# Performance work log

Hardware: AMD Instinct MI355X
Metric: run time of the kernel (lower is better)

Reference implementation:

```python
import jax, jax.numpy as jnp
import numpy as np

B, D, H, O, E = 16384, 256, 256, 256, 32
N_ACTIVE = 22          # int(32 * 0.7) from BoltzmannGate
TEMP = float(np.e)     # Boltzmann temperature
EPS = 1e-8


def setup_inputs() -> dict:
    key = jax.random.key(0)
    ks = jax.random.split(key, 7)
    s = 0.02  # init scale for weights
    return {
        "x":  jax.random.normal(ks[0], (B, D), dtype=jnp.float32),
        "W1": jax.random.normal(ks[1], (E, H, D), dtype=jnp.float32) * s,  # [E, out=H, in=D] torch Linear layout
        "b1": jax.random.normal(ks[2], (E, H), dtype=jnp.float32) * s,
        "W2": jax.random.normal(ks[3], (E, O, H), dtype=jnp.float32) * s,
        "b2": jax.random.normal(ks[4], (E, O), dtype=jnp.float32) * s,
        "Wg": jax.random.normal(ks[5], (E, D), dtype=jnp.float32) * s,
        "bg": jax.random.normal(ks[6], (E,), dtype=jnp.float32) * s,
    }


def reference(x, W1, b1, W2, b2, Wg, bg):
    # Dense all-experts forward: [B, E, H] -> relu -> [B, E, O]
    h = jax.nn.relu(jnp.einsum('bd,ehd->beh', x, W1) + b1[None, :, :])
    expert_out = jnp.einsum('beh,eoh->beo', h, W2) + b2[None, :, :]

    # Boltzmann gate: softmax(scores / T), keep top-k probs, renormalize.
    scores = (x @ Wg.T + bg) / TEMP                      # [B, E]
    probs = jax.nn.softmax(scores, axis=-1)
    _, topk_idx = jax.lax.top_k(probs, N_ACTIVE)         # [B, N_ACTIVE]
    mask = jnp.zeros_like(probs).at[jnp.arange(B)[:, None], topk_idx].set(1.0)
    weights = probs * mask
    weights = weights / (jnp.sum(weights, axis=-1, keepdims=True) + EPS)

    # Weighted combine over experts: [B, O]
    return jnp.einsum('be,beo->bo', weights, expert_out)
```

## Files before the change

### kernel.cpp

```cpp
#include <hip/hip_runtime.h>
#include <hip/hip_bf16.h>


typedef __attribute__((ext_vector_type(8))) short bf16x8;
typedef __attribute__((ext_vector_type(4))) float f32x4;

__device__ __forceinline__ unsigned short f2bf(float f) {
    unsigned u = __builtin_bit_cast(unsigned, f);
    u += 0x7FFFu + ((u >> 16) & 1u);
    return (unsigned short)(u >> 16);
}
__device__ __forceinline__ unsigned pack_bf16x2(float a, float b) {
    return (unsigned)f2bf(a) | ((unsigned)f2bf(b) << 16);
}

#define LX(r, ch) (((r) << 8) + ((((ch) ^ ((r) & 7))) << 3))

__global__ __launch_bounds__(256) void cvt_w(const float* __restrict__ W1,
                                             const float* __restrict__ W2,
                                             unsigned short* __restrict__ Wr) {
    int T = blockIdx.x * 256 + threadIdx.x;
    int lane = T & 63, t = (T >> 6) & 3, kb = (T >> 8) & 7;
    int g = (T >> 11) & 7, e = T >> 14;
    int l15 = lane & 15, quad = lane >> 4;
    int row = (g & 3) * 64 + t * 16 + l15;
    const float* src = ((g < 4) ? W1 : W2) +
                       ((long)e * 256 + row) * 256 + kb * 32 + quad * 8;
    float4 v0 = ((const float4*)src)[0], v1 = ((const float4*)src)[1];
    uint4 o;
    o.x = pack_bf16x2(v0.x, v0.y); o.y = pack_bf16x2(v0.z, v0.w);
    o.z = pack_bf16x2(v1.x, v1.y); o.w = pack_bf16x2(v1.z, v1.w);
    ((uint4*)Wr)[T] = o;
}

__global__ __launch_bounds__(512, 2) void moe_kernel(
    const float* __restrict__ x,
    const unsigned short* __restrict__ Wr,
    const float* __restrict__ bias1,
    const float* __restrict__ b2,
    const float* __restrict__ Wg,
    const float* __restrict__ bg,
    float* __restrict__ out)
{
    __shared__ __align__(16) unsigned short x_s[64 * 256];
    __shared__ __align__(16) unsigned short h_s[64 * 256];
    __shared__ float gws[64 * 33];

    const int tid  = threadIdx.x;
    const int wv   = tid >> 6, lane = tid & 63;
    const int quad = lane >> 4, l15 = lane & 15;
    const int crew = wv >> 2, g = wv & 3;
    const int row0 = blockIdx.x * 64;

#pragma unroll
    for (int c = 0; c < 4; ++c) {
        int chunk = tid + c * 512;
        int r = chunk >> 5, ch = chunk & 31;
        const float4* s = (const float4*)(x + (long)(row0 + r) * 256 + ch * 8);
        float4 v0 = s[0], v1 = s[1];
        uint4 o;
        o.x = pack_bf16x2(v0.x, v0.y); o.y = pack_bf16x2(v0.z, v0.w);
        o.z = pack_bf16x2(v1.x, v1.y); o.w = pack_bf16x2(v1.z, v1.w);
        *(uint4*)(&x_s[LX(r, ch)]) = o;
    }

    {
        const int e32 = lane & 31, half = lane >> 5;
        const float4* wg4 = (const float4*)(Wg + e32 * 256 + half * 128);
        float bgv = bg[e32];
        for (int i = 0; i < 8; ++i) {
            int lr = wv * 8 + i;
            const float4* xr4 = (const float4*)(x + (long)(row0 + lr) * 256 + half * 128);
            float acc = 0.f;
#pragma unroll
            for (int tt = 0; tt < 32; ++tt) {
                float4 w = wg4[tt], xv = xr4[tt];
                acc = fmaf(w.x, xv.x, acc); acc = fmaf(w.y, xv.y, acc);
                acc = fmaf(w.z, xv.z, acc); acc = fmaf(w.w, xv.w, acc);
            }
            acc += __shfl_xor(acc, 32);
            float score = (acc + bgv) / 2.71828182845904523f;

            float m = score;
#pragma unroll
            for (int d = 16; d >= 1; d >>= 1) m = fmaxf(m, __shfl_xor(m, d));
            float p = expf(score - m);
            float ps = p;
#pragma unroll
            for (int d = 16; d >= 1; d >>= 1) ps += __shfl_xor(ps, d);
            float prob = p / ps;

            int rank = 0;
#pragma unroll
            for (int j = 0; j < 32; ++j) {
                float pj = __shfl(prob, j);
                rank += (pj > prob || (pj == prob && j < e32)) ? 1 : 0;
            }
            float kept = (rank < 22) ? prob : 0.f;
            float wsum = kept;
#pragma unroll
            for (int d = 16; d >= 1; d >>= 1) wsum += __shfl_xor(wsum, d);
            float weight = kept / (wsum + 1e-8f);

            if (half == 0) gws[lr * 33 + e32] = weight;
        }
    }

    __syncthreads();

    f32x4 oacc[4][4];
#pragma unroll
    for (int ot = 0; ot < 4; ++ot)
#pragma unroll
        for (int rt = 0; rt < 4; ++rt) {
            f32x4 z = {0.f, 0.f, 0.f, 0.f};
            oacc[ot][rt] = z;
        }
    if (crew == 1) {
        for (int ee = 0; ee < 32; ++ee) {
            float gv[4];
#pragma unroll
            for (int rt = 0; rt < 4; ++rt) gv[rt] = gws[(rt * 16 + l15) * 33 + ee];
#pragma unroll
            for (int ot = 0; ot < 4; ++ot) {
                float4 bb = *(const float4*)(b2 + ee * 256 + g * 64 + ot * 16 + quad * 4);
#pragma unroll
                for (int rt = 0; rt < 4; ++rt) {
                    oacc[ot][rt][0] = fmaf(gv[rt], bb.x, oacc[ot][rt][0]);
                    oacc[ot][rt][1] = fmaf(gv[rt], bb.y, oacc[ot][rt][1]);
                    oacc[ot][rt][2] = fmaf(gv[rt], bb.z, oacc[ot][rt][2]);
                    oacc[ot][rt][3] = fmaf(gv[rt], bb.w, oacc[ot][rt][3]);
                }
            }
        }
    }

    bf16x8 buf[4];
    {
        const unsigned short* p0 = Wr + ((long)wv * 8) * 2048;
#pragma unroll
        for (int t = 0; t < 4; ++t)
            buf[t] = *(const bf16x8*)(p0 + t * 512 + lane * 8);
    }

    for (int e = 0; e <= 32; ++e) {
        f32x4 hacc[4][4];
        if (crew == 0) {
            if (e < 32) {
#pragma unroll
                for (int ht = 0; ht < 4; ++ht)
#pragma unroll
                    for (int rt = 0; rt < 4; ++rt) {
                        f32x4 z = {0.f, 0.f, 0.f, 0.f};
                        hacc[ht][rt] = z;
                    }
                const unsigned short* wcur = Wr + ((long)(e * 8 + wv) * 8) * 2048;
                const unsigned short* wnxt = Wr + ((long)((e + 1) * 8 + wv) * 8) * 2048;
#pragma unroll
                for (int kb = 0; kb < 8; ++kb) {
                    bf16x8 a[4];
#pragma unroll
                    for (int t = 0; t < 4; ++t) a[t] = buf[t];
                    const unsigned short* np = (kb < 7) ? (wcur + (kb + 1) * 2048) : wnxt;
#pragma unroll
                    for (int t = 0; t < 4; ++t)
                        buf[t] = *(const bf16x8*)(np + t * 512 + lane * 8);
                    bf16x8 bb[4];
#pragma unroll
                    for (int rt = 0; rt < 4; ++rt)
                        bb[rt] = *(const bf16x8*)(&x_s[LX(rt * 16 + l15, kb * 4 + quad)]);
#pragma unroll
                    for (int ht = 0; ht < 4; ++ht)
#pragma unroll
                        for (int rt = 0; rt < 4; ++rt)
                            hacc[ht][rt] = __builtin_amdgcn_mfma_f32_16x16x32_bf16(
                                a[ht], bb[rt], hacc[ht][rt], 0, 0, 0);
                }
            }
        } else {
            if (e >= 1) {
                const int me = e - 1;
                const unsigned short* wcur = Wr + ((long)(me * 8 + wv) * 8) * 2048;
                const unsigned short* wnxt = Wr + ((long)((me + 1) * 8 + wv) * 8) * 2048;
#pragma unroll
                for (int kb = 0; kb < 8; ++kb) {
                    bf16x8 a[4];
#pragma unroll
                    for (int t = 0; t < 4; ++t) a[t] = buf[t];
                    const unsigned short* np = (kb < 7) ? (wcur + (kb + 1) * 2048) : wnxt;
#pragma unroll
                    for (int t = 0; t < 4; ++t)
                        buf[t] = *(const bf16x8*)(np + t * 512 + lane * 8);
                    bf16x8 bb[4];
#pragma unroll
                    for (int rt = 0; rt < 4; ++rt)
                        bb[rt] = *(const bf16x8*)(&h_s[LX(rt * 16 + l15, kb * 4 + quad)]);
#pragma unroll
                    for (int ot = 0; ot < 4; ++ot)
#pragma unroll
                        for (int rt = 0; rt < 4; ++rt)
                            oacc[ot][rt] = __builtin_amdgcn_mfma_f32_16x16x32_bf16(
                                a[ot], bb[rt], oacc[ot][rt], 0, 0, 0);
                }
            }
        }

        __syncthreads();

        if (crew == 0 && e < 32) {
            float4 bv[4]; float gw[4];
#pragma unroll
            for (int ht = 0; ht < 4; ++ht)
                bv[ht] = *(const float4*)(bias1 + e * 256 + g * 64 + ht * 16 + quad * 4);
#pragma unroll
            for (int rt = 0; rt < 4; ++rt)
                gw[rt] = gws[(rt * 16 + l15) * 33 + e];
#pragma unroll
            for (int ht = 0; ht < 4; ++ht) {
                int hb = g * 64 + ht * 16 + quad * 4;
                int ch = hb >> 3, off = hb & 7;
#pragma unroll
                for (int rt = 0; rt < 4; ++rt) {
                    int r = rt * 16 + l15;
                    float v0 = fmaxf(hacc[ht][rt][0] + bv[ht].x, 0.f) * gw[rt];
                    float v1 = fmaxf(hacc[ht][rt][1] + bv[ht].y, 0.f) * gw[rt];
                    float v2 = fmaxf(hacc[ht][rt][2] + bv[ht].z, 0.f) * gw[rt];
                    float v3 = fmaxf(hacc[ht][rt][3] + bv[ht].w, 0.f) * gw[rt];
                    uint2 p;
                    p.x = pack_bf16x2(v0, v1);
                    p.y = pack_bf16x2(v2, v3);
                    *(uint2*)(&h_s[(r << 8) + ((ch ^ (r & 7)) << 3) + off]) = p;
                }
            }
        }

        __syncthreads();
    }

    if (crew == 1) {
#pragma unroll
        for (int ot = 0; ot < 4; ++ot)
#pragma unroll
            for (int rt = 0; rt < 4; ++rt)
                *(f32x4*)(out + (long)(row0 + rt * 16 + l15) * 256 +
                          g * 64 + ot * 16 + quad * 4) = oacc[ot][rt];
    }
}

extern "C" void kernel_launch(void* const* d_in, const int* in_sizes, int n_in,
                              void* d_out, int out_size, void* d_ws, size_t ws_size,
                              hipStream_t stream) {
    (void)in_sizes; (void)n_in; (void)out_size; (void)ws_size;
    const float* x  = (const float*)d_in[0];
    const float* W1 = (const float*)d_in[1];
    const float* b1 = (const float*)d_in[2];
    const float* W2 = (const float*)d_in[3];
    const float* b2 = (const float*)d_in[4];
    const float* Wg = (const float*)d_in[5];
    const float* bg = (const float*)d_in[6];
    float* out = (float*)d_out;

    unsigned short* Wr = (unsigned short*)d_ws;

    cvt_w<<<2048, 256, 0, stream>>>(W1, W2, Wr);
    moe_kernel<<<256, 512, 0, stream>>>(x, Wr, b1, b2, Wg, bg, out);
}
```

Measured before the change: 314.9 us.

## Double more waves per block, double-buffer h_s and drop one barrier per expert

Raises the block from 8 to 16 waves, splitting the 256 output columns across 8 waves per crew so each wave holds half the accumulators. The weight repack layout and the register prefetch change to match. h_s becomes double-buffered so the first-layer epilogue writes into the buffer for expert e while the second-layer crew reads expert e-1. This removes the second __syncthreads per expert iteration. It also adds s_setprio around the MFMA bursts. The risks are extra LDS (64KB+) limiting blocks per CU and the launch_bounds(1024,4) register cap forcing spills.

New measurement: 304.8 us. 3.2% less time.

```diff
diff --git a/kernel.cpp b/kernel.cpp
--- a/kernel.cpp
+++ b/kernel.cpp
@@ -20,11 +20,11 @@
                                              const float* __restrict__ W2,
                                              unsigned short* __restrict__ Wr) {
     int T = blockIdx.x * 256 + threadIdx.x;
-    int lane = T & 63, t = (T >> 6) & 3, kb = (T >> 8) & 7;
-    int g = (T >> 11) & 7, e = T >> 14;
+    int lane = T & 63, t = (T >> 6) & 1, kb = (T >> 7) & 7;
+    int s = (T >> 10) & 15, e = T >> 14;
     int l15 = lane & 15, quad = lane >> 4;
-    int row = (g & 3) * 64 + t * 16 + l15;
-    const float* src = ((g < 4) ? W1 : W2) +
+    int row = (s & 7) * 32 + t * 16 + l15;
+    const float* src = ((s < 8) ? W1 : W2) +
                        ((long)e * 256 + row) * 256 + kb * 32 + quad * 8;
     float4 v0 = ((const float4*)src)[0], v1 = ((const float4*)src)[1];
     uint4 o;
@@ -33,7 +33,7 @@
     ((uint4*)Wr)[T] = o;
 }
 
-__global__ __launch_bounds__(512, 2) void moe_kernel(
+__global__ __launch_bounds__(1024, 4) void moe_kernel(
     const float* __restrict__ x,
     const unsigned short* __restrict__ Wr,
     const float* __restrict__ bias1,
@@ -43,18 +43,18 @@
     float* __restrict__ out)
 {
     __shared__ __align__(16) unsigned short x_s[64 * 256];
-    __shared__ __align__(16) unsigned short h_s[64 * 256];
+    __shared__ __align__(16) unsigned short h_s[2][64 * 256];
     __shared__ float gws[64 * 33];
 
     const int tid  = threadIdx.x;
     const int wv   = tid >> 6, lane = tid & 63;
     const int quad = lane >> 4, l15 = lane & 15;
-    const int crew = wv >> 2, g = wv & 3;
+    const int crew = wv >> 3, g = wv & 7;
     const int row0 = blockIdx.x * 64;
 
 #pragma unroll
-    for (int c = 0; c < 4; ++c) {
-        int chunk = tid + c * 512;
+    for (int c = 0; c < 2; ++c) {
+        int chunk = tid + c * 1024;
         int r = chunk >> 5, ch = chunk & 31;
         const float4* s = (const float4*)(x + (long)(row0 + r) * 256 + ch * 8);
         float4 v0 = s[0], v1 = s[1];
@@ -68,8 +68,8 @@
         const int e32 = lane & 31, half = lane >> 5;
         const float4* wg4 = (const float4*)(Wg + e32 * 256 + half * 128);
         float bgv = bg[e32];
-        for (int i = 0; i < 8; ++i) {
-            int lr = wv * 8 + i;
+        for (int i = 0; i < 4; ++i) {
+            int lr = wv * 4 + i;
             const float4* xr4 = (const float4*)(x + (long)(row0 + lr) * 256 + half * 128);
             float acc = 0.f;
 #pragma unroll
@@ -108,9 +108,9 @@
 
     __syncthreads();
 
-    f32x4 oacc[4][4];
-#pragma unroll
-    for (int ot = 0; ot < 4; ++ot)
+    f32x4 oacc[2][4];
+#pragma unroll
+    for (int ot = 0; ot < 2; ++ot)
 #pragma unroll
         for (int rt = 0; rt < 4; ++rt) {
             f32x4 z = {0.f, 0.f, 0.f, 0.f};
@@ -122,8 +122,8 @@
 #pragma unroll
             for (int rt = 0; rt < 4; ++rt) gv[rt] = gws[(rt * 16 + l15) * 33 + ee];
 #pragma unroll
-            for (int ot = 0; ot < 4; ++ot) {
-                float4 bb = *(const float4*)(b2 + ee * 256 + g * 64 + ot * 16 + quad * 4);
+            for (int ot = 0; ot < 2; ++ot) {
+                float4 bb = *(const float4*)(b2 + ee * 256 + g * 32 + ot * 16 + quad * 4);
 #pragma unroll
                 for (int rt = 0; rt < 4; ++rt) {
                     oacc[ot][rt][0] = fmaf(gv[rt], bb.x, oacc[ot][rt][0]);
@@ -135,115 +135,113 @@
         }
     }
 
-    bf16x8 buf[4];
+    bf16x8 buf[2][2];
     {
-        const unsigned short* p0 = Wr + ((long)wv * 8) * 2048;
-#pragma unroll
-        for (int t = 0; t < 4; ++t)
-            buf[t] = *(const bf16x8*)(p0 + t * 512 + lane * 8);
+        const unsigned short* p0 = Wr + (long)wv * 8192;
+        buf[0][0] = *(const bf16x8*)(p0 + lane * 8);
+        buf[0][1] = *(const bf16x8*)(p0 + 512 + lane * 8);
+        buf[1][0] = *(const bf16x8*)(p0 + 1024 + lane * 8);
+        buf[1][1] = *(const bf16x8*)(p0 + 1536 + lane * 8);
     }
 
     for (int e = 0; e <= 32; ++e) {
-        f32x4 hacc[4][4];
         if (crew == 0) {
             if (e < 32) {
-#pragma unroll
-                for (int ht = 0; ht < 4; ++ht)
+                f32x4 hacc[2][4];
+#pragma unroll
+                for (int ht = 0; ht < 2; ++ht)
 #pragma unroll
                     for (int rt = 0; rt < 4; ++rt) {
                         f32x4 z = {0.f, 0.f, 0.f, 0.f};
                         hacc[ht][rt] = z;
                     }
-                const unsigned short* wcur = Wr + ((long)(e * 8 + wv) * 8) * 2048;
-                const unsigned short* wnxt = Wr + ((long)((e + 1) * 8 + wv) * 8) * 2048;
+                const unsigned short* w_e = Wr + ((long)(e * 16 + wv) * 8) * 1024;
 #pragma unroll
                 for (int kb = 0; kb < 8; ++kb) {
-                    bf16x8 a[4];
-#pragma unroll
-                    for (int t = 0; t < 4; ++t) a[t] = buf[t];
-                    const unsigned short* np = (kb < 7) ? (wcur + (kb + 1) * 2048) : wnxt;
-#pragma unroll
-                    for (int t = 0; t < 4; ++t)
-                        buf[t] = *(const bf16x8*)(np + t * 512 + lane * 8);
-                    bf16x8 bb[4];
+                    bf16x8 a0 = buf[kb & 1][0], a1 = buf[kb & 1][1];
+                    const unsigned short* np =
+                        w_e + ((kb < 6) ? (kb + 2) : (128 + kb - 6)) * 1024;
+                    buf[kb & 1][0] = *(const bf16x8*)(np + lane * 8);
+                    buf[kb & 1][1] = *(const bf16x8*)(np + 512 + lane * 8);
+                    bf16x8 bbv[4];
 #pragma unroll
                     for (int rt = 0; rt < 4; ++rt)
-                        bb[rt] = *(const bf16x8*)(&x_s[LX(rt * 16 + l15, kb * 4 + quad)]);
-#pragma unroll
-                    for (int ht = 0; ht < 4; ++ht)
-#pragma unroll
-                        for (int rt = 0; rt < 4; ++rt)
-                            hacc[ht][rt] = __builtin_amdgcn_mfma_f32_16x16x32_bf16(
-                                a[ht], bb[rt], hacc[ht][rt], 0, 0, 0);
+                        bbv[rt] = *(const bf16x8*)(&x_s[LX(rt * 16 + l15, kb * 4 + quad)]);
+                    __builtin_amdgcn_s_setprio(1);
+#pragma unroll
+                    for (int rt = 0; rt < 4; ++rt) {
+                        hacc[0][rt] = __builtin_amdgcn_mfma_f32_16x16x32_bf16(
+                            a0, bbv[rt], hacc[0][rt], 0, 0, 0);
+                        hacc[1][rt] = __builtin_amdgcn_mfma_f32_16x16x32_bf16(
+                            a1, bbv[rt], hacc[1][rt], 0, 0, 0);
+                    }
+                    __builtin_amdgcn_s_setprio(0);
+                }
+                unsigned short* hb = h_s[e & 1];
+                float4 bv[2]; float gw[4];
+#pragma unroll
+                for (int ht = 0; ht < 2; ++ht)
+                    bv[ht] = *(const float4*)(bias1 + e * 256 + g * 32 + ht * 16 + quad * 4);
+#pragma unroll
+                for (int rt = 0; rt < 4; ++rt)
+                    gw[rt] = gws[(rt * 16 + l15) * 33 + e];
+#pragma unroll
+                for (int ht = 0; ht < 2; ++ht) {
+                    int hcol = g * 32 + ht * 16 + quad * 4;
+                    int ch = hcol >> 3, off = hcol & 7;
+#pragma unroll
+                    for (int rt = 0; rt < 4; ++rt) {
+                        int r = rt * 16 + l15;
+                        float v0 = fmaxf(hacc[ht][rt][0] + bv[ht].x, 0.f) * gw[rt];
+                        float v1 = fmaxf(hacc[ht][rt][1] + bv[ht].y, 0.f) * gw[rt];
+                        float v2 = fmaxf(hacc[ht][rt][2] + bv[ht].z, 0.f) * gw[rt];
+                        float v3 = fmaxf(hacc[ht][rt][3] + bv[ht].w, 0.f) * gw[rt];
+                        uint2 pk;
+                        pk.x = pack_bf16x2(v0, v1);
+                        pk.y = pack_bf16x2(v2, v3);
+                        *(uint2*)(&hb[(r << 8) + ((ch ^ (r & 7)) << 3) + off]) = pk;
+                    }
                 }
             }
         } else {
             if (e >= 1) {
                 const int me = e - 1;
-                const unsigned short* wcur = Wr + ((long)(me * 8 + wv) * 8) * 2048;
-                const unsigned short* wnxt = Wr + ((long)((me + 1) * 8 + wv) * 8) * 2048;
+                const unsigned short* w_e = Wr + ((long)(me * 16 + wv) * 8) * 1024;
+                const unsigned short* hbuf = h_s[me & 1];
 #pragma unroll
                 for (int kb = 0; kb < 8; ++kb) {
-                    bf16x8 a[4];
-#pragma unroll
-                    for (int t = 0; t < 4; ++t) a[t] = buf[t];
-                    const unsigned short* np = (kb < 7) ? (wcur + (kb + 1) * 2048) : wnxt;
-#pragma unroll
-                    for (int t = 0; t < 4; ++t)
-                        buf[t] = *(const bf16x8*)(np + t * 512 + lane * 8);
-                    bf16x8 bb[4];
+                    bf16x8 a0 = buf[kb & 1][0], a1 = buf[kb & 1][1];
+                    const unsigned short* np =
+                        w_e + ((kb < 6) ? (kb + 2) : (128 + kb - 6)) * 1024;
+                    buf[kb & 1][0] = *(const bf16x8*)(np + lane * 8);
+                    buf[kb & 1][1] = *(const bf16x8*)(np + 512 + lane * 8);
+                    bf16x8 bbv[4];
 #pragma unroll
                     for (int rt = 0; rt < 4; ++rt)
-                        bb[rt] = *(const bf16x8*)(&h_s[LX(rt * 16 + l15, kb * 4 + quad)]);
-#pragma unroll
-                    for (int ot = 0; ot < 4; ++ot)
-#pragma unroll
-                        for (int rt = 0; rt < 4; ++rt)
-                            oacc[ot][rt] = __builtin_amdgcn_mfma_f32_16x16x32_bf16(
-                                a[ot], bb[rt], oacc[ot][rt], 0, 0, 0);
+                        bbv[rt] = *(const bf16x8*)(&hbuf[LX(rt * 16 + l15, kb * 4 + quad)]);
+                    __builtin_amdgcn_s_setprio(1);
+#pragma unroll
+                    for (int rt = 0; rt < 4; ++rt) {
+                        oacc[0][rt] = __builtin_amdgcn_mfma_f32_16x16x32_bf16(
+                            a0, bbv[rt], oacc[0][rt], 0, 0, 0);
+                        oacc[1][rt] = __builtin_amdgcn_mfma_f32_16x16x32_bf16(
+                            a1, bbv[rt], oacc[1][rt], 0, 0, 0);
+                    }
+                    __builtin_amdgcn_s_setprio(0);
                 }
             }
         }
 
         __syncthreads();
-
-        if (crew == 0 && e < 32) {
-            float4 bv[4]; float gw[4];
-#pragma unroll
-            for (int ht = 0; ht < 4; ++ht)
-                bv[ht] = *(const float4*)(bias1 + e * 256 + g * 64 + ht * 16 + quad * 4);
-#pragma unroll
-            for (int rt = 0; rt < 4; ++rt)
-                gw[rt] = gws[(rt * 16 + l15) * 33 + e];
-#pragma unroll
-            for (int ht = 0; ht < 4; ++ht) {
-                int hb = g * 64 + ht * 16 + quad * 4;
-                int ch = hb >> 3, off = hb & 7;
-#pragma unroll
-                for (int rt = 0; rt < 4; ++rt) {
-                    int r = rt * 16 + l15;
-                    float v0 = fmaxf(hacc[ht][rt][0] + bv[ht].x, 0.f) * gw[rt];
-                    float v1 = fmaxf(hacc[ht][rt][1] + bv[ht].y, 0.f) * gw[rt];
-                    float v2 = fmaxf(hacc[ht][rt][2] + bv[ht].z, 0.f) * gw[rt];
-                    float v3 = fmaxf(hacc[ht][rt][3] + bv[ht].w, 0.f) * gw[rt];
-                    uint2 p;
-                    p.x = pack_bf16x2(v0, v1);
-                    p.y = pack_bf16x2(v2, v3);
-                    *(uint2*)(&h_s[(r << 8) + ((ch ^ (r & 7)) << 3) + off]) = p;
-                }
-            }
-        }
-
-        __syncthreads();
     }
 
     if (crew == 1) {
 #pragma unroll
-        for (int ot = 0; ot < 4; ++ot)
+        for (int ot = 0; ot < 2; ++ot)
 #pragma unroll
             for (int rt = 0; rt < 4; ++rt)
                 *(f32x4*)(out + (long)(row0 + rt * 16 + l15) * 256 +
-                          g * 64 + ot * 16 + quad * 4) = oacc[ot][rt];
+                          g * 32 + ot * 16 + quad * 4) = oacc[ot][rt];
     }
 }
 
@@ -263,5 +261,5 @@
     unsigned short* Wr = (unsigned short*)d_ws;
 
     cvt_w<<<2048, 256, 0, stream>>>(W1, W2, Wr);
-    moe_kernel<<<256, 512, 0, stream>>>(x, Wr, b1, b2, Wg, bg, out);
-}
+    moe_kernel<<<256, 1024, 0, stream>>>(x, Wr, b1, b2, Wg, bg, out);
+}
```
